# Kernel tuning notes

Measured on AMD Instinct MI355X. Metric: run time of the kernel, lower is better.

## Reference

```python
import jax, jax.numpy as jnp
import numpy as np

N, D_IN, D_HID, D_OUT, E = 100000, 128, 256, 64, 1600000


def setup_inputs() -> dict:
    key = jax.random.key(0)
    ks = jax.random.split(key, 6)
    x = jax.random.normal(ks[0], (N, D_IN), dtype=jnp.float32)
    edge_index = jax.random.randint(ks[1], (2, E), 0, N, dtype=jnp.int64)
    # Linear params (PyTorch convention: y = x @ W.T + b)
    W1 = jax.random.normal(ks[2], (D_HID, D_IN), dtype=jnp.float32) / np.sqrt(D_IN)
    b1 = jax.random.normal(ks[3], (D_HID,), dtype=jnp.float32) * 0.01
    W2 = jax.random.normal(ks[4], (D_OUT, D_HID), dtype=jnp.float32) / np.sqrt(D_HID)
    b2 = jax.random.normal(ks[5], (D_OUT,), dtype=jnp.float32) * 0.01
    return {"x": x, "edge_index": edge_index, "W1": W1, "b1": b1, "W2": W2, "b2": b2}


def _scatter_mean(vals, dst, num_nodes):
    # sum neighbor features per destination node, divide by in-degree (0-degree -> 0)
    s = jax.ops.segment_sum(vals, dst, num_segments=num_nodes)
    cnt = jax.ops.segment_sum(jnp.ones((dst.shape[0],), vals.dtype), dst, num_segments=num_nodes)
    return s / jnp.maximum(cnt, 1.0)[:, None]


def _sage_layer(x, src, dst, W, b):
    neighbors = x[src]                      # [E, d] gather
    agg = _scatter_mean(neighbors, dst, x.shape[0])  # [N, d]
    return agg @ W.T + b


def reference(x, edge_index, W1, b1, W2, b2):
    src, dst = edge_index[0], edge_index[1]
    h = _sage_layer(x, src, dst, W1, b1)
    h = jax.nn.relu(h)
    # dropout is identity at inference (training=False)
    y = _sage_layer(h, src, dst, W2, b2)
    return jax.nn.log_softmax(y, axis=1)
```

## Files before the change

### kernel.cpp

```cpp
#include <hip/hip_runtime.h>


typedef __attribute__((ext_vector_type(8))) short bf16x8;
typedef __attribute__((ext_vector_type(4))) float f32x4;
typedef __attribute__((ext_vector_type(2))) float f32x2;

#define BSHIFT 10
#define BMASK  1023
#define SRCMASK 0x1FFFF
#define TBIN   4096

#if __has_builtin(__builtin_amdgcn_cvt_pk_f32_fp8) && __has_builtin(__builtin_amdgcn_cvt_pk_fp8_f32)
#define HAVE_FP8_CVT 1
#else
#define HAVE_FP8_CVT 0
#endif

__device__ inline ushort f2bf(float f) {
  union { float f; unsigned u; } c; c.f = f;
  unsigned r = (c.u + 0x7fffu + ((c.u >> 16) & 1u)) >> 16;
  return (ushort)r;
}
__device__ inline float bf2f(ushort u) {
  union { unsigned u; float f; } c; c.u = ((unsigned)u) << 16;
  return c.f;
}

#if HAVE_FP8_CVT
template <bool HI>
__device__ inline f32x2 fp8x2f(unsigned w) {
  return __builtin_amdgcn_cvt_pk_f32_fp8((int)w, HI);
}
template <bool HI>
__device__ inline unsigned fp8pack2(unsigned old, float a, float b) {
  return (unsigned)__builtin_amdgcn_cvt_pk_fp8_f32(a, b, (int)old, HI);
}
#else
__device__ inline float fp8tof_1(unsigned b) {
  unsigned e = (b >> 3) & 15u, m = b & 7u;
  float v;
  if (e == 0) v = (float)m * 0x1p-9f;
  else { union { unsigned u; float f; } c; c.u = ((e + 120u) << 23) | (m << 20); v = c.f; }
  return (b & 0x80u) ? -v : v;
}
template <bool HI>
__device__ inline f32x2 fp8x2f(unsigned w) {
  unsigned sh = HI ? 16 : 0;
  f32x2 r;
  r.x = fp8tof_1((w >> sh) & 0xFFu);
  r.y = fp8tof_1((w >> (sh + 8)) & 0xFFu);
  return r;
}
__device__ inline unsigned f2fp8_1(float f) {
  float af = fabsf(f);
  unsigned s = (f < 0.f) ? 0x80u : 0u;
  if (!(af < 448.f)) return s | 0x7Eu;
  if (af < 0x1p-6f) {
    int m = (int)rintf(af * 512.0f);
    if (m >= 8) return s | 0x08u;
    return s | (unsigned)m;
  }
  int e;
  frexpf(af, &e);
  int E = e - 1;
  int q = (int)rintf(ldexpf(af, 3 - E));
  if (q >= 16) { q = 8; E += 1; if (E > 8) return s | 0x7Eu; }
  return s | ((unsigned)(E + 7) << 3) | ((unsigned)q & 7u);
}
template <bool HI>
__device__ inline unsigned fp8pack2(unsigned old, float a, float b) {
  unsigned pair = f2fp8_1(a) | (f2fp8_1(b) << 8);
  return HI ? ((old & 0x0000FFFFu) | (pair << 16)) : ((old & 0xFFFF0000u) | pair);
}
#endif

__global__ void __launch_bounds__(64) k_detect(const int* __restrict__ ei, int* __restrict__ flag) {
  int t = threadIdx.x;
  int v = ei[2 * t + 1];
  unsigned long long m = __ballot(v != 0);
  if (t == 0) *flag = (m == 0ull) ? 1 : 0;
}

__global__ void __launch_bounds__(256) k_prep_x(const float4* __restrict__ x4, uint2* __restrict__ xq8, int total8) {
  int i = blockIdx.x * 256 + threadIdx.x;
  if (i >= total8) return;
  float4 v0 = x4[2 * i], v1 = x4[2 * i + 1];
  unsigned w0 = fp8pack2<false>(0u, v0.x, v0.y);
  w0 = fp8pack2<true>(w0, v0.z, v0.w);
  unsigned w1 = fp8pack2<false>(0u, v1.x, v1.y);
  w1 = fp8pack2<true>(w1, v1.z, v1.w);
  xq8[i] = make_uint2(w0, w1);
}

__global__ void __launch_bounds__(256) k_prep_w(const float* __restrict__ W1, const float* __restrict__ W2,
                                                ushort* __restrict__ W1f, ushort* __restrict__ W2f) {
  int idx = blockIdx.x * 256 + threadIdx.x;
  if (idx < 32768) {
    int jt = idx >> 11, rem = idx & 2047;
    int kt = rem >> 9, rem2 = rem & 511;
    int l = rem2 >> 3, e = rem2 & 7;
    int k = kt * 32 + (l >> 4) * 8 + e;
    int j = jt * 16 + (l & 15);
    W1f[idx] = f2bf(W1[j * 128 + k]);
  } else {
    int i2 = idx - 32768;
    if (i2 < 16384) {
      int ot = i2 >> 12, rem = i2 & 4095;
      int kt = rem >> 9;
      int l = (rem >> 3) & 63, e = rem & 7;
      int k = kt * 32 + (l >> 4) * 8 + e;
      int o = ot * 16 + (l & 15);
      W2f[i2] = f2bf(W2[o * 256 + k]);
    }
  }
}

__global__ void __launch_bounds__(256) k_bhist(const int* __restrict__ ei, const int* __restrict__ flag,
                                               int* __restrict__ bcnt, int E, int NB) {
  __shared__ int h[128];
  int t = threadIdx.x;
  if (t < 128) h[t] = 0;
  __syncthreads();
  bool f64 = (*flag != 0);
  int stride = gridDim.x * 256;
  for (int e = blockIdx.x * 256 + t; e < E; e += stride) {
    int d;
    if (f64) d = (int)((const long long*)ei)[(size_t)E + e];
    else     d = ei[(size_t)E + e];
    atomicAdd(&h[d >> BSHIFT], 1);
  }
  __syncthreads();
  if (t < NB && h[t]) atomicAdd(&bcnt[t], h[t]);
}

__global__ void __launch_bounds__(128) k_bscan(const int* __restrict__ bcnt, int* __restrict__ bbase,
                                               int* __restrict__ bcur, int* __restrict__ row_ptr,
                                               int NB, int N, int E) {
  __shared__ int s[128];
  int t = threadIdx.x;
  int v = (t < NB) ? bcnt[t] : 0;
  s[t] = v;
  __syncthreads();
  for (int o = 1; o < 128; o <<= 1) {
    int u = (t >= o) ? s[t - o] : 0;
    __syncthreads();
    s[t] += u;
    __syncthreads();
  }
  if (t < NB) {
    int base = s[t] - v;
    bbase[t] = base;
    bcur[t] = base;
  }
  if (t == 0) {
    bbase[NB] = E;
    row_ptr[N] = E;
  }
}

__global__ void __launch_bounds__(256) k_bin(const int* __restrict__ ei, const int* __restrict__ flag,
                                             int* __restrict__ bcur, int* __restrict__ gpair, int E, int NB) {
  __shared__ int hist[128], base[128], segb[128], cur[128], scanb[128];
  __shared__ int ent[TBIN];
  __shared__ int gdx[TBIN];
  int t = threadIdx.x;
  int e0 = blockIdx.x * TBIN;
  int cnt = E - e0; if (cnt > TBIN) cnt = TBIN;
  if (t < 128) hist[t] = 0;
  __syncthreads();
  bool f64 = (*flag != 0);
  int ment[16], mbk[16];
#pragma unroll
  for (int i = 0; i < 16; ++i) {
    int idx = t + i * 256;
    mbk[i] = -1;
    if (idx < cnt) {
      int e = e0 + idx;
      int s, d;
      if (f64) {
        const long long* p = (const long long*)ei;
        s = (int)p[e];
        d = (int)p[(size_t)E + e];
      } else {
        s = ei[e];
        d = ei[(size_t)E + e];
      }
      int b = d >> BSHIFT;
      mbk[i] = b;
      ment[i] = ((d & BMASK) << 17) | s;
      atomicAdd(&hist[b], 1);
    }
  }
  __syncthreads();
  if (t < 128) scanb[t] = hist[t];
  __syncthreads();
  for (int o = 1; o < 128; o <<= 1) {
    int u = 0;
    if (t < 128 && t >= o) u = scanb[t - o];
    __syncthreads();
    if (t < 128) scanb[t] += u;
    __syncthreads();
  }
  if (t < 128) {
    int b0 = scanb[t] - hist[t];
    base[t] = b0;
    cur[t] = b0;
    segb[t] = (t < NB && hist[t] > 0) ? atomicAdd(&bcur[t], hist[t]) : 0;
  }
  __syncthreads();
#pragma unroll
  for (int i = 0; i < 16; ++i) {
    int b = mbk[i];
    if (b >= 0) {
      int pos = atomicAdd(&cur[b], 1);
      ent[pos] = ment[i];
      gdx[pos] = segb[b] + (pos - base[b]);
    }
  }
  __syncthreads();
  for (int i = t; i < cnt; i += 256) gpair[gdx[i]] = ent[i];
}

__global__ void __launch_bounds__(1024) k_bcsr(const int* __restrict__ gpair, const int* __restrict__ bbase,
                                               int* __restrict__ row_ptr, float* __restrict__ inv_deg,
                                               int* __restrict__ csr, int N) {
  __shared__ int hist[1024], pre[1024], cur[1024];
  int b = blockIdx.x, t = threadIdx.x;
  int start = bbase[b], end = bbase[b + 1];
  hist[t] = 0;
  __syncthreads();
  for (int i = start + t; i < end; i += 1024) {
    int e = gpair[i];
    atomicAdd(&hist[e >> 17], 1);
  }
  __syncthreads();
  pre[t] = hist[t];
  __syncthreads();
  for (int o = 1; o < 1024; o <<= 1) {
    int u = (t >= o) ? pre[t - o] : 0;
    __syncthreads();
    pre[t] += u;
    __syncthreads();
  }
  int gbase = start + pre[t] - hist[t];
  int n = (b << BSHIFT) + t;
  if (n < N) {
    row_ptr[n] = gbase;
    inv_deg[n] = 1.0f / (float)(hist[t] > 0 ? hist[t] : 1);
  }
  cur[t] = gbase;
  __syncthreads();
  for (int i = start + t; i < end; i += 1024) {
    int e = gpair[i];
    int pos = atomicAdd(&cur[e >> 17], 1);
    csr[pos] = e & SRCMASK;
  }
}

__global__ void __launch_bounds__(256) k_agg1(const unsigned char* __restrict__ xq, const int* __restrict__ csr,
                                              const int* __restrict__ row_ptr, const float* __restrict__ inv_deg,
                                              ushort* __restrict__ agg1b, int N) {
  int n = blockIdx.x * 4 + (threadIdx.x >> 6);
  if (n >= N) return;
  int lane = threadIdx.x & 63;
  int half = lane >> 5, p = lane & 31;
  int s = row_ptr[n], e = row_ptr[n + 1];
  f32x2 a0 = (f32x2)(0.f), a1 = (f32x2)(0.f);

  for (int base = s; base < e; base += 64) {
    int cnt = e - base; if (cnt > 64) cnt = 64;
    int ci = csr[base + (lane < cnt ? lane : cnt - 1)];
    int j = 0;
    for (; j + 7 < cnt; j += 8) {
      int i0 = __shfl(ci, j + half);
      int i1 = __shfl(ci, j + 2 + half);
      int i2 = __shfl(ci, j + 4 + half);
      int i3 = __shfl(ci, j + 6 + half);
      unsigned w0 = *(const unsigned*)(xq + (size_t)i0 * 128 + p * 4);
      unsigned w1 = *(const unsigned*)(xq + (size_t)i1 * 128 + p * 4);
      unsigned w2 = *(const unsigned*)(xq + (size_t)i2 * 128 + p * 4);
      unsigned w3 = *(const unsigned*)(xq + (size_t)i3 * 128 + p * 4);
      a0 += fp8x2f<false>(w0); a1 += fp8x2f<true>(w0);
      a0 += fp8x2f<false>(w1); a1 += fp8x2f<true>(w1);
      a0 += fp8x2f<false>(w2); a1 += fp8x2f<true>(w2);
      a0 += fp8x2f<false>(w3); a1 += fp8x2f<true>(w3);
    }
    for (; j + 1 < cnt; j += 2) {
      int i0 = __shfl(ci, j + half);
      unsigned w0 = *(const unsigned*)(xq + (size_t)i0 * 128 + p * 4);
      a0 += fp8x2f<false>(w0); a1 += fp8x2f<true>(w0);
    }
    if (j < cnt) {
      int i0 = __shfl(ci, j);
      unsigned w0 = *(const unsigned*)(xq + (size_t)i0 * 128 + p * 4);
      if (half == 0) { a0 += fp8x2f<false>(w0); a1 += fp8x2f<true>(w0); }
    }
  }
  a0.x += __shfl_xor(a0.x, 32); a0.y += __shfl_xor(a0.y, 32);
  a1.x += __shfl_xor(a1.x, 32); a1.y += __shfl_xor(a1.y, 32);
  if (half == 0) {
    float inv = inv_deg[n];
    ushort4 o;
    o.x = f2bf(a0.x * inv); o.y = f2bf(a0.y * inv);
    o.z = f2bf(a1.x * inv); o.w = f2bf(a1.y * inv);
    *(ushort4*)(agg1b + (size_t)n * 128 + p * 4) = o;
  }
}

__global__ void __launch_bounds__(256) k_mlp(const ushort* __restrict__ agg1b, const bf16x8* __restrict__ w1f,
                                             const float* __restrict__ b1, const bf16x8* __restrict__ w2f,
                                             unsigned char* __restrict__ gq, int N) {
  __shared__ __align__(16) ushort sm[16896];
  ushort* aT = sm;
  ushort* hT = sm;
  const int t = threadIdx.x;
  const int n0 = blockIdx.x * 64;

#pragma unroll
  for (int i = 0; i < 4; ++i) {
    int idx = i * 256 + t;
    int row = idx >> 4, c8 = idx & 15;
    int rr = n0 + row; if (rr >= N) rr = N - 1;
    bf16x8 v = *(const bf16x8*)(agg1b + (size_t)rr * 128 + c8 * 8);
    *(bf16x8*)(aT + row * 136 + c8 * 8) = v;
  }
  __syncthreads();

  const int w = t >> 6, l = t & 63;
  const int lm = l & 15, lq = l >> 4;

  f32x4 acc[4][4];
#pragma unroll
  for (int mt = 0; mt < 4; ++mt)
#pragma unroll
    for (int nt = 0; nt < 4; ++nt) acc[mt][nt] = (f32x4)(0.f);

#pragma unroll
  for (int kt = 0; kt < 4; ++kt) {
    bf16x8 b[4], a[4];
#pragma unroll
    for (int nt = 0; nt < 4; ++nt)
      b[nt] = w1f[((w * 4 + nt) * 4 + kt) * 64 + l];
#pragma unroll
    for (int mt = 0; mt < 4; ++mt)
      a[mt] = *(const bf16x8*)(aT + (mt * 16 + lm) * 136 + kt * 32 + lq * 8);
#pragma unroll
    for (int mt = 0; mt < 4; ++mt)
#pragma unroll
      for (int nt = 0; nt < 4; ++nt)
        acc[mt][nt] = __builtin_amdgcn_mfma_f32_16x16x32_bf16(a[mt], b[nt], acc[mt][nt], 0, 0, 0);
  }
  __syncthreads();

#pragma unroll
  for (int nt = 0; nt < 4; ++nt) {
    int col = w * 64 + nt * 16 + lm;
    float bb = b1[col];
#pragma unroll
    for (int mt = 0; mt < 4; ++mt)
#pragma unroll
      for (int r = 0; r < 4; ++r) {
        int row = mt * 16 + lq * 4 + r;
        float hv = acc[mt][nt][r] + bb;
        hT[row * 264 + col] = f2bf(fmaxf(hv, 0.f));
      }
  }
  __syncthreads();

  f32x4 acc2[4];
#pragma unroll
  for (int ot = 0; ot < 4; ++ot) acc2[ot] = (f32x4)(0.f);
#pragma unroll
  for (int kt = 0; kt < 8; ++kt) {
    bf16x8 a2 = *(const bf16x8*)(hT + (w * 16 + lm) * 264 + kt * 32 + lq * 8);
#pragma unroll
    for (int ot = 0; ot < 4; ++ot) {
      bf16x8 bf = w2f[(ot * 8 + kt) * 64 + l];
      acc2[ot] = __builtin_amdgcn_mfma_f32_16x16x32_bf16(a2, bf, acc2[ot], 0, 0, 0);
    }
  }
#pragma unroll
  for (int ot = 0; ot < 4; ++ot)
#pragma unroll
    for (int r = 0; r < 4; ++r) {
      int row = n0 + w * 16 + lq * 4 + r;
      if (row < N) {
        unsigned pw = fp8pack2<false>(0u, acc2[ot][r], acc2[ot][r]);
        gq[(size_t)row * 64 + ot * 16 + lm] = (unsigned char)(pw & 0xFFu);
      }
    }
}

__global__ void __launch_bounds__(256) k_agg2(const unsigned char* __restrict__ gq, const int* __restrict__ csr,
                                              const int* __restrict__ row_ptr, const float* __restrict__ inv_deg,
                                              const float* __restrict__ b2, float* __restrict__ out, int N) {
  int n = blockIdx.x * 4 + (threadIdx.x >> 6);
  if (n >= N) return;
  int lane = threadIdx.x & 63;
  int q = lane >> 4, p = lane & 15;
  int s = row_ptr[n], e = row_ptr[n + 1];
  f32x2 a0 = (f32x2)(0.f), a1 = (f32x2)(0.f);

  for (int base = s; base < e; base += 64) {
    int cnt = e - base; if (cnt > 64) cnt = 64;
    int ci = csr[base + (lane < cnt ? lane : cnt - 1)];
    int j = 0;
    for (; j + 15 < cnt; j += 16) {
      int i0 = __shfl(ci, j + q);
      int i1 = __shfl(ci, j + 4 + q);
      int i2 = __shfl(ci, j + 8 + q);
      int i3 = __shfl(ci, j + 12 + q);
      unsigned w0 = *(const unsigned*)(gq + (size_t)i0 * 64 + p * 4);
      unsigned w1 = *(const unsigned*)(gq + (size_t)i1 * 64 + p * 4);
      unsigned w2 = *(const unsigned*)(gq + (size_t)i2 * 64 + p * 4);
      unsigned w3 = *(const unsigned*)(gq + (size_t)i3 * 64 + p * 4);
      a0 += fp8x2f<false>(w0); a1 += fp8x2f<true>(w0);
      a0 += fp8x2f<false>(w1); a1 += fp8x2f<true>(w1);
      a0 += fp8x2f<false>(w2); a1 += fp8x2f<true>(w2);
      a0 += fp8x2f<false>(w3); a1 += fp8x2f<true>(w3);
    }
    for (; j + 3 < cnt; j += 4) {
      int i0 = __shfl(ci, j + q);
      unsigned w0 = *(const unsigned*)(gq + (size_t)i0 * 64 + p * 4);
      a0 += fp8x2f<false>(w0); a1 += fp8x2f<true>(w0);
    }
    if (j < cnt) {
      int sel = j + q;
      int i0 = __shfl(ci, sel < cnt ? sel : j);
      unsigned w0 = *(const unsigned*)(gq + (size_t)i0 * 64 + p * 4);
      if (sel < cnt) { a0 += fp8x2f<false>(w0); a1 += fp8x2f<true>(w0); }
    }
  }
  a0.x += __shfl_xor(a0.x, 16); a0.y += __shfl_xor(a0.y, 16);
  a1.x += __shfl_xor(a1.x, 16); a1.y += __shfl_xor(a1.y, 16);
  a0.x += __shfl_xor(a0.x, 32); a0.y += __shfl_xor(a0.y, 32);
  a1.x += __shfl_xor(a1.x, 32); a1.y += __shfl_xor(a1.y, 32);
  float inv = inv_deg[n];
  float4 b = *(const float4*)(b2 + p * 4);
  float4 v;
  v.x = a0.x * inv + b.x;
  v.y = a0.y * inv + b.y;
  v.z = a1.x * inv + b.z;
  v.w = a1.y * inv + b.w;
  float mx = fmaxf(fmaxf(v.x, v.y), fmaxf(v.z, v.w));
#pragma unroll
  for (int off = 1; off <= 8; off <<= 1) mx = fmaxf(mx, __shfl_xor(mx, off));
  float se = expf(v.x - mx) + expf(v.y - mx) + expf(v.z - mx) + expf(v.w - mx);
#pragma unroll
  for (int off = 1; off <= 8; off <<= 1) se += __shfl_xor(se, off);
  float lse = mx + logf(se);
  v.x -= lse; v.y -= lse; v.z -= lse; v.w -= lse;
  if (q == 0) *(float4*)(out + (size_t)n * 64 + p * 4) = v;
}

extern "C" void kernel_launch(void* const* d_in, const int* in_sizes, int n_in,
                              void* d_out, int out_size, void* d_ws, size_t ws_size,
                              hipStream_t stream) {
  const float* x  = (const float*)d_in[0];
  const int*   ei = (const int*)d_in[1];
  const float* W1 = (const float*)d_in[2];
  const float* b1 = (const float*)d_in[3];
  const float* W2 = (const float*)d_in[4];
  const float* b2 = (const float*)d_in[5];
  float* out = (float*)d_out;
  const int N = in_sizes[0] / 128;
  const int E = in_sizes[1] / 2;
  const int NB = (N + BMASK) >> BSHIFT;

  char* base = (char*)d_ws;
  size_t off = 0;
  auto alloc = [&](size_t bytes) -> char* {
    char* p = base + off;
    off += (bytes + 255) & ~(size_t)255;
    return p;
  };
  int*    flag    = (int*)alloc(4);
  int*    bcnt    = (int*)alloc((size_t)NB * 4);
  int*    bbase   = (int*)alloc((size_t)(NB + 1) * 4);
  int*    bcur    = (int*)alloc((size_t)NB * 4);
  int*    gpair   = (int*)alloc((size_t)E * 4);
  int*    row_ptr = (int*)alloc((size_t)(N + 1) * 4);
  float*  inv_deg = (float*)alloc((size_t)N * 4);
  int*    csr     = (int*)alloc((size_t)E * 4);
  unsigned char* xq = (unsigned char*)alloc((size_t)N * 128);
  ushort* W1f     = (ushort*)alloc((size_t)32768 * 2);
  ushort* W2f     = (ushort*)alloc((size_t)16384 * 2);
  ushort* agg1b   = (ushort*)alloc((size_t)N * 128 * 2);
  unsigned char* gq = (unsigned char*)alloc((size_t)N * 64);
  (void)ws_size; (void)n_in; (void)out_size;

  hipMemsetAsync(bcnt, 0, (size_t)NB * 4, stream);
  k_detect<<<1, 64, 0, stream>>>(ei, flag);
  k_prep_x<<<(N * 16 + 255) / 256, 256, 0, stream>>>((const float4*)x, (uint2*)xq, N * 16);
  k_prep_w<<<192, 256, 0, stream>>>(W1, W2, W1f, W2f);
  k_bhist<<<512, 256, 0, stream>>>(ei, flag, bcnt, E, NB);
  k_bscan<<<1, 128, 0, stream>>>(bcnt, bbase, bcur, row_ptr, NB, N, E);
  k_bin<<<(E + TBIN - 1) / TBIN, 256, 0, stream>>>(ei, flag, bcur, gpair, E, NB);
  k_bcsr<<<NB, 1024, 0, stream>>>(gpair, bbase, row_ptr, inv_deg, csr, N);
  k_agg1<<<(N + 3) / 4, 256, 0, stream>>>(xq, csr, row_ptr, inv_deg, agg1b, N);
  k_mlp<<<(N + 63) / 64, 256, 0, stream>>>(agg1b, (const bf16x8*)W1f, b1, (const bf16x8*)W2f, gq, N);
  k_agg2<<<(N + 3) / 4, 256, 0, stream>>>(gq, csr, row_ptr, inv_deg, b2, out, N);
}
```

Measured before the change: 283.0 us.

## Process four nodes per wavefront in both aggregation kernels

Both gather-aggregate kernels now assign four destination nodes to each 64-lane wavefront, with 16 lanes per node, instead of one node per wavefront. Each lane loads wider vectors (8 bytes in the first aggregation) and the cross-half shuffle reductions are gone. Row pointers are fetched once per wave and shared by shuffle, and neighbours are walked in masked chunks of 16 up to the wave's largest degree. This cuts wasted lanes and per-node overhead on low-degree nodes (average degree about 16), at the cost of divergence when degrees within a group differ and extra masked loads.

```diff
diff --git a/kernel.cpp b/kernel.cpp
--- a/kernel.cpp
+++ b/kernel.cpp
@@ -260,50 +260,54 @@
 __global__ void __launch_bounds__(256) k_agg1(const unsigned char* __restrict__ xq, const int* __restrict__ csr,
                                               const int* __restrict__ row_ptr, const float* __restrict__ inv_deg,
                                               ushort* __restrict__ agg1b, int N) {
-  int n = blockIdx.x * 4 + (threadIdx.x >> 6);
-  if (n >= N) return;
-  int lane = threadIdx.x & 63;
-  int half = lane >> 5, p = lane & 31;
-  int s = row_ptr[n], e = row_ptr[n + 1];
-  f32x2 a0 = (f32x2)(0.f), a1 = (f32x2)(0.f);
-
-  for (int base = s; base < e; base += 64) {
-    int cnt = e - base; if (cnt > 64) cnt = 64;
-    int ci = csr[base + (lane < cnt ? lane : cnt - 1)];
-    int j = 0;
-    for (; j + 7 < cnt; j += 8) {
-      int i0 = __shfl(ci, j + half);
-      int i1 = __shfl(ci, j + 2 + half);
-      int i2 = __shfl(ci, j + 4 + half);
-      int i3 = __shfl(ci, j + 6 + half);
-      unsigned w0 = *(const unsigned*)(xq + (size_t)i0 * 128 + p * 4);
-      unsigned w1 = *(const unsigned*)(xq + (size_t)i1 * 128 + p * 4);
-      unsigned w2 = *(const unsigned*)(xq + (size_t)i2 * 128 + p * 4);
-      unsigned w3 = *(const unsigned*)(xq + (size_t)i3 * 128 + p * 4);
-      a0 += fp8x2f<false>(w0); a1 += fp8x2f<true>(w0);
-      a0 += fp8x2f<false>(w1); a1 += fp8x2f<true>(w1);
-      a0 += fp8x2f<false>(w2); a1 += fp8x2f<true>(w2);
-      a0 += fp8x2f<false>(w3); a1 += fp8x2f<true>(w3);
-    }
-    for (; j + 1 < cnt; j += 2) {
-      int i0 = __shfl(ci, j + half);
-      unsigned w0 = *(const unsigned*)(xq + (size_t)i0 * 128 + p * 4);
-      a0 += fp8x2f<false>(w0); a1 += fp8x2f<true>(w0);
-    }
-    if (j < cnt) {
-      int i0 = __shfl(ci, j);
-      unsigned w0 = *(const unsigned*)(xq + (size_t)i0 * 128 + p * 4);
-      if (half == 0) { a0 += fp8x2f<false>(w0); a1 += fp8x2f<true>(w0); }
-    }
-  }
-  a0.x += __shfl_xor(a0.x, 32); a0.y += __shfl_xor(a0.y, 32);
-  a1.x += __shfl_xor(a1.x, 32); a1.y += __shfl_xor(a1.y, 32);
-  if (half == 0) {
-    float inv = inv_deg[n];
-    ushort4 o;
-    o.x = f2bf(a0.x * inv); o.y = f2bf(a0.y * inv);
-    o.z = f2bf(a1.x * inv); o.w = f2bf(a1.y * inv);
-    *(ushort4*)(agg1b + (size_t)n * 128 + p * 4) = o;
+  const int lane = threadIdx.x & 63;
+  const int g = lane >> 4, p = lane & 15;
+  const int n0 = (blockIdx.x * 4 + (threadIdx.x >> 6)) * 4;
+  if (n0 >= N) return;
+  const int n = n0 + g;
+  int rpidx = n0 + (lane < 4 ? lane : 4);
+  if (rpidx > N) rpidx = N;
+  const int rv = row_ptr[rpidx];
+  const int s = __shfl(rv, g);
+  const int cnt = __shfl(rv, g + 1) - s;
+  const float inv = inv_deg[n < N ? n : 0];
+  int maxc = cnt;
+  maxc = max(maxc, __shfl_xor(maxc, 16));
+  maxc = max(maxc, __shfl_xor(maxc, 32));
+
+  f32x2 a0 = (f32x2)(0.f), a1 = (f32x2)(0.f), a2 = (f32x2)(0.f), a3 = (f32x2)(0.f);
+  for (int base = 0; base < maxc; base += 16) {
+    int li = base + p, cm = cnt - 1;
+    if (li > cm) li = cm;
+    if (li < 0) li = 0;
+    int ci = 0;
+    if (cnt > 0) ci = csr[s + li];
+#pragma unroll
+    for (int u = 0; u < 8; ++u) {
+      int idx = __shfl(ci, (lane & 48) + u);
+      uint2 wv = *(const uint2*)(xq + (size_t)idx * 128 + p * 8);
+      if (base + u >= cnt) { wv.x = 0u; wv.y = 0u; }
+      a0 += fp8x2f<false>(wv.x); a1 += fp8x2f<true>(wv.x);
+      a2 += fp8x2f<false>(wv.y); a3 += fp8x2f<true>(wv.y);
+    }
+    if (base + 8 < maxc) {
+#pragma unroll
+      for (int u = 8; u < 16; ++u) {
+        int idx = __shfl(ci, (lane & 48) + u);
+        uint2 wv = *(const uint2*)(xq + (size_t)idx * 128 + p * 8);
+        if (base + u >= cnt) { wv.x = 0u; wv.y = 0u; }
+        a0 += fp8x2f<false>(wv.x); a1 += fp8x2f<true>(wv.x);
+        a2 += fp8x2f<false>(wv.y); a3 += fp8x2f<true>(wv.y);
+      }
+    }
+  }
+  if (n < N) {
+    bf16x8 o;
+    o[0] = (short)f2bf(a0.x * inv); o[1] = (short)f2bf(a0.y * inv);
+    o[2] = (short)f2bf(a1.x * inv); o[3] = (short)f2bf(a1.y * inv);
+    o[4] = (short)f2bf(a2.x * inv); o[5] = (short)f2bf(a2.y * inv);
+    o[6] = (short)f2bf(a3.x * inv); o[7] = (short)f2bf(a3.y * inv);
+    *(bf16x8*)(agg1b + (size_t)n * 128 + p * 8) = o;
   }
 }
 
@@ -394,63 +398,62 @@
 __global__ void __launch_bounds__(256) k_agg2(const unsigned char* __restrict__ gq, const int* __restrict__ csr,
                                               const int* __restrict__ row_ptr, const float* __restrict__ inv_deg,
                                               const float* __restrict__ b2, float* __restrict__ out, int N) {
-  int n = blockIdx.x * 4 + (threadIdx.x >> 6);
-  if (n >= N) return;
-  int lane = threadIdx.x & 63;
-  int q = lane >> 4, p = lane & 15;
-  int s = row_ptr[n], e = row_ptr[n + 1];
+  const int lane = threadIdx.x & 63;
+  const int g = lane >> 4, p = lane & 15;
+  const int n0 = (blockIdx.x * 4 + (threadIdx.x >> 6)) * 4;
+  if (n0 >= N) return;
+  const int n = n0 + g;
+  int rpidx = n0 + (lane < 4 ? lane : 4);
+  if (rpidx > N) rpidx = N;
+  const int rv = row_ptr[rpidx];
+  const int s = __shfl(rv, g);
+  const int cnt = __shfl(rv, g + 1) - s;
+  const float inv = inv_deg[n < N ? n : 0];
+  const float4 bv = *(const float4*)(b2 + p * 4);
+  int maxc = cnt;
+  maxc = max(maxc, __shfl_xor(maxc, 16));
+  maxc = max(maxc, __shfl_xor(maxc, 32));
+
   f32x2 a0 = (f32x2)(0.f), a1 = (f32x2)(0.f);
-
-  for (int base = s; base < e; base += 64) {
-    int cnt = e - base; if (cnt > 64) cnt = 64;
-    int ci = csr[base + (lane < cnt ? lane : cnt - 1)];
-    int j = 0;
-    for (; j + 15 < cnt; j += 16) {
-      int i0 = __shfl(ci, j + q);
-      int i1 = __shfl(ci, j + 4 + q);
-      int i2 = __shfl(ci, j + 8 + q);
-      int i3 = __shfl(ci, j + 12 + q);
-      unsigned w0 = *(const unsigned*)(gq + (size_t)i0 * 64 + p * 4);
-      unsigned w1 = *(const unsigned*)(gq + (size_t)i1 * 64 + p * 4);
-      unsigned w2 = *(const unsigned*)(gq + (size_t)i2 * 64 + p * 4);
-      unsigned w3 = *(const unsigned*)(gq + (size_t)i3 * 64 + p * 4);
-      a0 += fp8x2f<false>(w0); a1 += fp8x2f<true>(w0);
-      a0 += fp8x2f<false>(w1); a1 += fp8x2f<true>(w1);
-      a0 += fp8x2f<false>(w2); a1 += fp8x2f<true>(w2);
-      a0 += fp8x2f<false>(w3); a1 += fp8x2f<true>(w3);
-    }
-    for (; j + 3 < cnt; j += 4) {
-      int i0 = __shfl(ci, j + q);
-      unsigned w0 = *(const unsigned*)(gq + (size_t)i0 * 64 + p * 4);
-      a0 += fp8x2f<false>(w0); a1 += fp8x2f<true>(w0);
-    }
-    if (j < cnt) {
-      int sel = j + q;
-      int i0 = __shfl(ci, sel < cnt ? sel : j);
-      unsigned w0 = *(const unsigned*)(gq + (size_t)i0 * 64 + p * 4);
-      if (sel < cnt) { a0 += fp8x2f<false>(w0); a1 += fp8x2f<true>(w0); }
-    }
-  }
-  a0.x += __shfl_xor(a0.x, 16); a0.y += __shfl_xor(a0.y, 16);
-  a1.x += __shfl_xor(a1.x, 16); a1.y += __shfl_xor(a1.y, 16);
-  a0.x += __shfl_xor(a0.x, 32); a0.y += __shfl_xor(a0.y, 32);
-  a1.x += __shfl_xor(a1.x, 32); a1.y += __shfl_xor(a1.y, 32);
-  float inv = inv_deg[n];
-  float4 b = *(const float4*)(b2 + p * 4);
-  float4 v;
-  v.x = a0.x * inv + b.x;
-  v.y = a0.y * inv + b.y;
-  v.z = a1.x * inv + b.z;
-  v.w = a1.y * inv + b.w;
-  float mx = fmaxf(fmaxf(v.x, v.y), fmaxf(v.z, v.w));
+  for (int base = 0; base < maxc; base += 16) {
+    int li = base + p, cm = cnt - 1;
+    if (li > cm) li = cm;
+    if (li < 0) li = 0;
+    int ci = 0;
+    if (cnt > 0) ci = csr[s + li];
+#pragma unroll
+    for (int u = 0; u < 8; ++u) {
+      int idx = __shfl(ci, (lane & 48) + u);
+      unsigned wv = *(const unsigned*)(gq + (size_t)idx * 64 + p * 4);
+      if (base + u >= cnt) wv = 0u;
+      a0 += fp8x2f<false>(wv); a1 += fp8x2f<true>(wv);
+    }
+    if (base + 8 < maxc) {
+#pragma unroll
+      for (int u = 8; u < 16; ++u) {
+        int idx = __shfl(ci, (lane & 48) + u);
+        unsigned wv = *(const unsigned*)(gq + (size_t)idx * 64 + p * 4);
+        if (base + u >= cnt) wv = 0u;
+        a0 += fp8x2f<false>(wv); a1 += fp8x2f<true>(wv);
+      }
+    }
+  }
+  float vx = a0.x * inv + bv.x;
+  float vy = a0.y * inv + bv.y;
+  float vz = a1.x * inv + bv.z;
+  float vw = a1.y * inv + bv.w;
+  float mx = fmaxf(fmaxf(vx, vy), fmaxf(vz, vw));
 #pragma unroll
   for (int off = 1; off <= 8; off <<= 1) mx = fmaxf(mx, __shfl_xor(mx, off));
-  float se = expf(v.x - mx) + expf(v.y - mx) + expf(v.z - mx) + expf(v.w - mx);
+  float se = expf(vx - mx) + expf(vy - mx) + expf(vz - mx) + expf(vw - mx);
 #pragma unroll
   for (int off = 1; off <= 8; off <<= 1) se += __shfl_xor(se, off);
   float lse = mx + logf(se);
-  v.x -= lse; v.y -= lse; v.z -= lse; v.w -= lse;
-  if (q == 0) *(float4*)(out + (size_t)n * 64 + p * 4) = v;
+  if (n < N) {
+    float4 o;
+    o.x = vx - lse; o.y = vy - lse; o.z = vz - lse; o.w = vw - lse;
+    *(float4*)(out + (size_t)n * 64 + p * 4) = o;
+  }
 }
 
 extern "C" void kernel_launch(void* const* d_in, const int* in_sizes, int n_in,
@@ -497,7 +500,7 @@
   k_bscan<<<1, 128, 0, stream>>>(bcnt, bbase, bcur, row_ptr, NB, N, E);
   k_bin<<<(E + TBIN - 1) / TBIN, 256, 0, stream>>>(ei, flag, bcur, gpair, E, NB);
   k_bcsr<<<NB, 1024, 0, stream>>>(gpair, bbase, row_ptr, inv_deg, csr, N);
-  k_agg1<<<(N + 3) / 4, 256, 0, stream>>>(xq, csr, row_ptr, inv_deg, agg1b, N);
+  k_agg1<<<(N + 15) / 16, 256, 0, stream>>>(xq, csr, row_ptr, inv_deg, agg1b, N);
   k_mlp<<<(N + 63) / 64, 256, 0, stream>>>(agg1b, (const bf16x8*)W1f, b1, (const bf16x8*)W2f, gq, N);
-  k_agg2<<<(N + 3) / 4, 256, 0, stream>>>(gq, csr, row_ptr, inv_deg, b2, out, N);
-}
+  k_agg2<<<(N + 15) / 16, 256, 0, stream>>>(gq, csr, row_ptr, inv_deg, b2, out, N);
+}
```

Result: no change. 282.8 us (-0.1%).
